# Kernel tuning notes

Hardware: AMD Instinct MI355X
Metric: run time of the kernel (lower is better)

## Reference

```python
import jax, jax.numpy as jnp
from jax import lax
import numpy as np

N_ASSETS = 128
BATCH = 2048
MAX_WEIGHT = 1.0
N_ITERS = 300      # projected-gradient iterations (unrolled solver)
N_BISECT = 40      # bisection steps for simplex-box projection
LR = 0.02
EPS = 1e-8


def project_capped_simplex(v, c):
    """Project rows of v onto {w : sum(w)=1, -c <= w <= c} via bisection on the
    shift tau in w = clip(v - tau, -c, c). sum is decreasing in tau."""
    lo = jnp.min(v, axis=-1, keepdims=True) - c - 1.0
    hi = jnp.max(v, axis=-1, keepdims=True) + c

    def body(carry, _):
        lo, hi = carry
        mid = 0.5 * (lo + hi)
        s = jnp.sum(jnp.clip(v - mid, -c, c), axis=-1, keepdims=True)
        too_big = s > 1.0
        return (jnp.where(too_big, mid, lo), jnp.where(too_big, hi, mid)), None

    (lo, hi), _ = lax.scan(body, (lo, hi), None, length=N_BISECT)
    tau = 0.5 * (lo + hi)
    return jnp.clip(v - tau, -c, c)


def solve_markowitz(rets, A, alpha_abs, max_weight):
    """maximize r.w - sqrt(w'Aw) - alpha*||w||_2  s.t. sum w = 1, |w| <= c,
    via projected gradient ascent (fixed iteration count, fully batched)."""
    B, n = rets.shape
    w0 = jnp.full((B, n), 1.0 / n, dtype=rets.dtype)
    a = alpha_abs[:, None]

    def step(w, _):
        Aw = jnp.einsum('bij,bj->bi', A, w)                       # (B,n)
        risk = jnp.sqrt(jnp.sum(w * Aw, axis=-1, keepdims=True) + EPS)
        nrm = jnp.sqrt(jnp.sum(w * w, axis=-1, keepdims=True) + EPS)
        g = rets - Aw / risk - a * (w / nrm)                      # gradient of objective
        w_new = project_capped_simplex(w + LR * g, max_weight)
        return w_new, None

    w, _ = lax.scan(step, w0, None, length=N_ITERS)
    return w


def setup_inputs() -> dict:
    key = jax.random.key(0)
    k1, k2, k3, k4 = jax.random.split(key, 4)
    rets = 0.05 * jax.random.normal(k1, (BATCH, N_ASSETS), dtype=jnp.float32)
    # PSD covariance: B B^T / n + jitter*I
    Bm = jax.random.normal(k2, (BATCH, N_ASSETS, N_ASSETS), dtype=jnp.float32)
    covmat = jnp.einsum('bik,bjk->bij', Bm, Bm) / N_ASSETS
    covmat = covmat + 1e-3 * jnp.eye(N_ASSETS, dtype=jnp.float32)
    gamma = jax.random.uniform(k3, (BATCH,), dtype=jnp.float32, minval=0.1, maxval=2.0)
    alpha = jax.random.normal(k4, (BATCH,), dtype=jnp.float32)
    return {"rets": rets, "covmat": covmat, "gamma": gamma, "alpha": alpha}


def reference(rets, covmat, gamma, alpha):
    alpha_abs = jnp.abs(alpha)
    A = gamma[:, None, None] * covmat   # gamma-adjusted covariance, as in forward
    return solve_markowitz(rets, A, alpha_abs, MAX_WEIGHT)
```

## Files before the change

### kernel.cpp

```cpp
#include <hip/hip_runtime.h>
#include <math.h>

#define NA      128
#define NBATCH  2048
#define NTHR    256
#define NIT     300
#define NBIS    40
#define LRC     0.02f
#define EPSC    1e-8f

template <int CTRL>
__device__ __forceinline__ float dpp_sum_step(float x) {
  int s = __builtin_amdgcn_update_dpp(0, __float_as_int(x), CTRL, 0xF, 0xF, true);
  return x + __int_as_float(s);
}
__device__ __forceinline__ float wave_sum64(float x) {
  x = dpp_sum_step<0x111>(x);
  x = dpp_sum_step<0x112>(x);
  x = dpp_sum_step<0x114>(x);
  x = dpp_sum_step<0x118>(x);
  x = dpp_sum_step<0x142>(x);
  x = dpp_sum_step<0x143>(x);
  return x;
}
template <int CTRL>
__device__ __forceinline__ float dpp_mov_self(float x) {
  int s = __builtin_amdgcn_update_dpp(__float_as_int(x), __float_as_int(x), CTRL, 0xF, 0xF, false);
  return __int_as_float(s);
}
__device__ __forceinline__ float wave_min64(float x) {
  x = fminf(x, dpp_mov_self<0x111>(x));
  x = fminf(x, dpp_mov_self<0x112>(x));
  x = fminf(x, dpp_mov_self<0x114>(x));
  x = fminf(x, dpp_mov_self<0x118>(x));
  x = fminf(x, dpp_mov_self<0x142>(x));
  x = fminf(x, dpp_mov_self<0x143>(x));
  return x;
}
__device__ __forceinline__ float wave_max64(float x) {
  x = fmaxf(x, dpp_mov_self<0x111>(x));
  x = fmaxf(x, dpp_mov_self<0x112>(x));
  x = fmaxf(x, dpp_mov_self<0x114>(x));
  x = fmaxf(x, dpp_mov_self<0x118>(x));
  x = fmaxf(x, dpp_mov_self<0x142>(x));
  x = fmaxf(x, dpp_mov_self<0x143>(x));
  return x;
}
__device__ __forceinline__ float read_lane63(float x) {
  return __int_as_float(__builtin_amdgcn_readlane(__float_as_int(x), 63));
}
__device__ __forceinline__ float clip1(float x) {
  return __builtin_amdgcn_fmed3f(x, -1.0f, 1.0f);
}

__global__ __launch_bounds__(NTHR)
__attribute__((amdgpu_waves_per_eu(1, 4)))
void markowitz_kernel(
    const float* __restrict__ rets,
    const float* __restrict__ covmat,
    const float* __restrict__ gamma,
    const float* __restrict__ alpha,
    float* __restrict__ out)
{
  const int b    = blockIdx.x;
  const int tid  = threadIdx.x;
  const int r    = tid & (NA - 1);
  const int h    = tid >> 7;
  const int lane = tid & 63;
  const int wv   = tid >> 6;

  __shared__ __align__(16) float ws[NA];
  __shared__ __align__(16) float vs[NA];
  __shared__ float partial[NTHR];
  __shared__ float pp[8];
  __shared__ float tau_s;

  const float gm = gamma[b];
  const float4* Ar = reinterpret_cast<const float4*>(
      covmat + (size_t)b * NA * NA + (size_t)r * NA + (size_t)h * 64);
  float4 a[16];
#pragma unroll
  for (int k = 0; k < 16; ++k) {
    float4 q = Ar[k];
    a[k] = make_float4(q.x * gm, q.y * gm, q.z * gm, q.w * gm);
  }
  const float r_t = rets[b * NA + r];
  const float av  = fabsf(alpha[b]);

  float w_t = 1.0f / NA;
  if (tid < NA) ws[tid] = w_t;
  __syncthreads();

  float v_t = 0.0f;

#pragma unroll 1
  for (int it = 0; it < NIT; ++it) {
    const float4* ws4 = reinterpret_cast<const float4*>(ws) + 16 * h;
    float4 acc = make_float4(0.f, 0.f, 0.f, 0.f);
#pragma unroll
    for (int k = 0; k < 16; ++k) {
      float4 wk = ws4[k];
      acc.x = fmaf(a[k].x, wk.x, acc.x);
      acc.y = fmaf(a[k].y, wk.y, acc.y);
      acc.z = fmaf(a[k].z, wk.z, acc.z);
      acc.w = fmaf(a[k].w, wk.w, acc.w);
    }
    partial[tid] = (acc.x + acc.y) + (acc.z + acc.w);
    __syncthreads();

    float Aw = 0.0f;
    if (tid < NA) {
      Aw = partial[tid] + partial[tid + NA];
      float p1 = wave_sum64(w_t * Aw);
      float p2 = wave_sum64(w_t * w_t);
      if (lane == 63) { pp[wv * 2 + 0] = p1; pp[wv * 2 + 1] = p2; }
    }
    __syncthreads();

    if (tid < NA) {
      const float risk = sqrtf(pp[0] + pp[2] + EPSC);
      const float nrm  = sqrtf(pp[1] + pp[3] + EPSC);
      const float g_t  = r_t - Aw / risk - av * (w_t / nrm);
      v_t = w_t + LRC * g_t;
      vs[tid] = v_t;
      float mn = wave_min64(v_t);
      float mx = wave_max64(v_t);
      if (lane == 63) { pp[4 + wv] = mn; pp[6 + wv] = mx; }
    }
    __syncthreads();

    if (wv == 0) {
      float v0 = vs[lane];
      float v1 = vs[lane + 64];
      float lo = fminf(pp[4], pp[5]) - 2.0f;
      float hi = fmaxf(pp[6], pp[7]) + 1.0f;
#pragma unroll 1
      for (int rr = 0; rr < NBIS; ++rr) {
        const float mid = 0.5f * (lo + hi);
        float s = clip1(v0 - mid) + clip1(v1 - mid);
        s = wave_sum64(s);
        const float stot = read_lane63(s);
        const bool big = stot > 1.0f;
        lo = big ? mid : lo;
        hi = big ? hi : mid;
      }
      if (lane == 0) tau_s = 0.5f * (lo + hi);
    }
    __syncthreads();

    if (tid < NA) {
      w_t = clip1(v_t - tau_s);
      ws[tid] = w_t;
    }
    __syncthreads();
  }

  if (tid < NA) out[b * NA + tid] = w_t;
}

extern "C" void kernel_launch(void* const* d_in, const int* in_sizes, int n_in,
                              void* d_out, int out_size, void* d_ws, size_t ws_size,
                              hipStream_t stream) {
  const float* rets   = (const float*)d_in[0];
  const float* covmat = (const float*)d_in[1];
  const float* gamma  = (const float*)d_in[2];
  const float* alpha  = (const float*)d_in[3];
  float* out = (float*)d_out;

  hipLaunchKernelGGL(markowitz_kernel, dim3(NBATCH), dim3(NTHR), 0, stream,
                     rets, covmat, gamma, alpha, out);
}
```

Measured before the change: 2.726 ms.

## Split matvec four ways across 512 threads and fold projection writeback into bisection wave

The block grows to 512 threads, so each thread holds a quarter-row of the covariance (8 float4 registers instead of 16) and the matvec partials are reduced four ways. The min/max reduction moves into the single bisection wave, which now also writes the projected weights directly, removing one barrier and the tau broadcast per iteration. The bisection wave is rotated by block index so the serial chain lands on different SIMDs across blocks. The cost is more idle threads and longer barriers per block in exchange for fewer registers and possibly higher occupancy.

```diff
diff --git a/kernel.cpp b/kernel.cpp
--- a/kernel.cpp
+++ b/kernel.cpp
@@ -3,7 +3,7 @@
 
 #define NA      128
 #define NBATCH  2048
-#define NTHR    256
+#define NTHR    512
 #define NIT     300
 #define NBIS    40
 #define LRC     0.02f
@@ -46,7 +46,7 @@
   x = fmaxf(x, dpp_mov_self<0x143>(x));
   return x;
 }
-__device__ __forceinline__ float read_lane63(float x) {
+__device__ __forceinline__ float bcast63(float x) {
   return __int_as_float(__builtin_amdgcn_readlane(__float_as_int(x), 63));
 }
 __device__ __forceinline__ float clip1(float x) {
@@ -54,7 +54,6 @@
 }
 
 __global__ __launch_bounds__(NTHR)
-__attribute__((amdgpu_waves_per_eu(1, 4)))
 void markowitz_kernel(
     const float* __restrict__ rets,
     const float* __restrict__ covmat,
@@ -65,54 +64,51 @@
   const int b    = blockIdx.x;
   const int tid  = threadIdx.x;
   const int r    = tid & (NA - 1);
-  const int h    = tid >> 7;
+  const int q    = tid >> 7;
   const int lane = tid & 63;
   const int wv   = tid >> 6;
+  const int chain_wv = b & 7;
 
   __shared__ __align__(16) float ws[NA];
   __shared__ __align__(16) float vs[NA];
-  __shared__ float partial[NTHR];
-  __shared__ float pp[8];
-  __shared__ float tau_s;
+  __shared__ __align__(16) float part[NTHR];
+  __shared__ float pp[4];
 
   const float gm = gamma[b];
-  const float4* Ar = reinterpret_cast<const float4*>(
-      covmat + (size_t)b * NA * NA + (size_t)r * NA + (size_t)h * 64);
-  float4 a[16];
+  const float4* Aq = reinterpret_cast<const float4*>(
+      covmat + (size_t)b * NA * NA + (size_t)r * NA + (size_t)q * 32);
+  float4 a[8];
 #pragma unroll
-  for (int k = 0; k < 16; ++k) {
-    float4 q = Ar[k];
-    a[k] = make_float4(q.x * gm, q.y * gm, q.z * gm, q.w * gm);
+  for (int k = 0; k < 8; ++k) {
+    float4 t = Aq[k];
+    a[k] = make_float4(t.x * gm, t.y * gm, t.z * gm, t.w * gm);
   }
-  const float r_t = rets[b * NA + r];
-  const float av  = fabsf(alpha[b]);
-
-  float w_t = 1.0f / NA;
-  if (tid < NA) ws[tid] = w_t;
+  const float av = fabsf(alpha[b]);
+  float r_c = 0.0f;
+  if (tid < NA) { r_c = rets[b * NA + tid]; ws[tid] = 1.0f / NA; }
   __syncthreads();
-
-  float v_t = 0.0f;
 
 #pragma unroll 1
   for (int it = 0; it < NIT; ++it) {
-    const float4* ws4 = reinterpret_cast<const float4*>(ws) + 16 * h;
+    const float4* w4 = reinterpret_cast<const float4*>(ws) + q * 8;
     float4 acc = make_float4(0.f, 0.f, 0.f, 0.f);
 #pragma unroll
-    for (int k = 0; k < 16; ++k) {
-      float4 wk = ws4[k];
+    for (int k = 0; k < 8; ++k) {
+      float4 wk = w4[k];
       acc.x = fmaf(a[k].x, wk.x, acc.x);
       acc.y = fmaf(a[k].y, wk.y, acc.y);
       acc.z = fmaf(a[k].z, wk.z, acc.z);
       acc.w = fmaf(a[k].w, wk.w, acc.w);
     }
-    partial[tid] = (acc.x + acc.y) + (acc.z + acc.w);
+    part[tid] = (acc.x + acc.y) + (acc.z + acc.w);
     __syncthreads();
 
-    float Aw = 0.0f;
+    float Aw = 0.f, w_c = 0.f, v_c = 0.f;
     if (tid < NA) {
-      Aw = partial[tid] + partial[tid + NA];
-      float p1 = wave_sum64(w_t * Aw);
-      float p2 = wave_sum64(w_t * w_t);
+      Aw  = (part[tid] + part[tid + NA]) + (part[tid + 2 * NA] + part[tid + 3 * NA]);
+      w_c = ws[tid];
+      float p1 = wave_sum64(w_c * Aw);
+      float p2 = wave_sum64(w_c * w_c);
       if (lane == 63) { pp[wv * 2 + 0] = p1; pp[wv * 2 + 1] = p2; }
     }
     __syncthreads();
@@ -120,42 +116,36 @@
     if (tid < NA) {
       const float risk = sqrtf(pp[0] + pp[2] + EPSC);
       const float nrm  = sqrtf(pp[1] + pp[3] + EPSC);
-      const float g_t  = r_t - Aw / risk - av * (w_t / nrm);
-      v_t = w_t + LRC * g_t;
-      vs[tid] = v_t;
-      float mn = wave_min64(v_t);
-      float mx = wave_max64(v_t);
-      if (lane == 63) { pp[4 + wv] = mn; pp[6 + wv] = mx; }
+      const float g    = r_c - Aw / risk - av * (w_c / nrm);
+      v_c = w_c + LRC * g;
+      vs[tid] = v_c;
     }
     __syncthreads();
 
-    if (wv == 0) {
+    if (wv == chain_wv) {
       float v0 = vs[lane];
       float v1 = vs[lane + 64];
-      float lo = fminf(pp[4], pp[5]) - 2.0f;
-      float hi = fmaxf(pp[6], pp[7]) + 1.0f;
+      float mn = bcast63(wave_min64(fminf(v0, v1)));
+      float mx = bcast63(wave_max64(fmaxf(v0, v1)));
+      float lo = mn - 2.0f;
+      float hi = mx + 1.0f;
 #pragma unroll 1
       for (int rr = 0; rr < NBIS; ++rr) {
         const float mid = 0.5f * (lo + hi);
-        float s = clip1(v0 - mid) + clip1(v1 - mid);
-        s = wave_sum64(s);
-        const float stot = read_lane63(s);
-        const bool big = stot > 1.0f;
+        float s = wave_sum64(clip1(v0 - mid) + clip1(v1 - mid));
+        const float st = bcast63(s);
+        const bool big = st > 1.0f;
         lo = big ? mid : lo;
         hi = big ? hi : mid;
       }
-      if (lane == 0) tau_s = 0.5f * (lo + hi);
-    }
-    __syncthreads();
-
-    if (tid < NA) {
-      w_t = clip1(v_t - tau_s);
-      ws[tid] = w_t;
+      const float tau = 0.5f * (lo + hi);
+      ws[lane]      = clip1(v0 - tau);
+      ws[lane + 64] = clip1(v1 - tau);
     }
     __syncthreads();
   }
 
-  if (tid < NA) out[b * NA + tid] = w_t;
+  if (tid < NA) out[b * NA + tid] = ws[tid];
 }
 
 extern "C" void kernel_launch(void* const* d_in, const int* in_sizes, int n_in,
```

New measurement: 2.685 ms. About the same (-1.5%).
